# Kernel optimization log

Hardware: AMD Instinct MI355X
Metric: run time of the kernel (lower is better)

## Reference

```python
import jax, jax.numpy as jnp
import numpy as np

B, C, H, W, K = 8, 768, 64, 64, 256
EPS = 1e-12  # torch F.normalize eps


def setup_inputs() -> dict:
    key = jax.random.key(0)
    k1, k2 = jax.random.split(key)
    return {
        "x": jax.random.normal(k1, (B, C, H, W), dtype=jnp.float32),
        "centroids": jax.random.normal(k2, (B, C, K), dtype=jnp.float32),
        "sim_alpha": jnp.ones((1,), dtype=jnp.float32),
        "sim_beta": jnp.zeros((1,), dtype=jnp.float32),
    }


def reference(x, centroids, sim_alpha, sim_beta):
    b, c, h, w = x.shape
    n = h * w
    x_r = x.reshape(b, c, n)               # (B,C,N)
    xt = jnp.swapaxes(x_r, 1, 2)           # (B,N,C) tokens
    ct = jnp.swapaxes(centroids, 1, 2)     # (B,K,C) centroids
    # cosine similarity (F.normalize uses max(norm, eps))
    xn = xt / jnp.maximum(jnp.linalg.norm(xt, axis=-1, keepdims=True), EPS)
    cn = ct / jnp.maximum(jnp.linalg.norm(ct, axis=-1, keepdims=True), EPS)
    cos = jnp.einsum('bkc,bnc->bkn', cn, xn)                  # (B,K,N)
    sim = jax.nn.sigmoid(sim_beta + sim_alpha * cos)          # (B,K,N)
    # hard assignment mask: each token kept only for its argmax centroid
    max_idx = jnp.argmax(sim, axis=1)                         # (B,N)
    mask = jnp.swapaxes(jax.nn.one_hot(max_idx, sim.shape[1], dtype=sim.dtype), 1, 2)  # (B,K,N)
    sim_masked = sim * mask                                   # (B,K,N)
    # aggregation: sum over tokens weighted by masked similarity
    agg = jnp.einsum('bkn,bnc->bkc', sim_masked, xt)          # (B,K,C)
    counts = jnp.sum(mask, axis=-1, keepdims=True)            # (B,K,1)
    hyperedges = (agg + ct) / (counts + 1.0)                  # (B,K,C)
    return hyperedges, sim_masked
```

## Files before the change

kernel.cpp:

```cpp
#include <hip/hip_runtime.h>
#include <cmath>

#define Bdim 8
#define Cdim 768
#define Kdim 256
#define Ndim 4096
#define NT 64
#define KC2 32
#define NCH (Cdim / KC2)

typedef __bf16 bf16x8 __attribute__((ext_vector_type(8)));
typedef short  s16x8  __attribute__((ext_vector_type(8)));
typedef float  f32x4  __attribute__((ext_vector_type(4)));
union U8 { s16x8 s; bf16x8 b; };

typedef __attribute__((address_space(1))) const unsigned int g_u32;
typedef __attribute__((address_space(3))) unsigned int l_u32;
__device__ __forceinline__ void gload16(const void* g, void* l) {
    __builtin_amdgcn_global_load_lds((g_u32*)g, (l_u32*)l, 16, 0, 0);
}

__device__ __forceinline__ unsigned short bf16_rne(float f) {
    unsigned u = __float_as_uint(f);
    unsigned r = u + 0x7FFFu + ((u >> 16) & 1u);
    return (unsigned short)(r >> 16);
}
__device__ __forceinline__ float bf2f(unsigned short h) {
    return __uint_as_float((unsigned)h << 16);
}

__device__ __forceinline__ void split3(float v, short& h, short& m, short& l) {
    unsigned u = __float_as_uint(v);
    unsigned th = u + 0x7FFFu + ((u >> 16) & 1u);
    h = (short)(th >> 16);
    float r1 = v - __uint_as_float(th & 0xFFFF0000u);
    unsigned u1 = __float_as_uint(r1);
    unsigned tm = u1 + 0x7FFFu + ((u1 >> 16) & 1u);
    m = (short)(tm >> 16);
    float r2 = r1 - __uint_as_float(tm & 0xFFFF0000u);
    unsigned u2 = __float_as_uint(r2);
    unsigned tl = u2 + 0x7FFFu + ((u2 >> 16) & 1u);
    l = (short)(tl >> 16);
}

__global__ __launch_bounds__(256) void prep_kernel(
    const float* __restrict__ cents, float* __restrict__ invc, int* __restrict__ cnt)
{
    __shared__ float red[4][Kdim];
    const int tid = threadIdx.x;
    const int b = blockIdx.x;
    const float* cb = cents + (size_t)b * Cdim * Kdim;
    const int q = tid & 63, g = tid >> 6;
    float4 ss = make_float4(0.f, 0.f, 0.f, 0.f);
    for (int r = g; r < Cdim; r += 4) {
        float4 v = *(const float4*)(cb + (size_t)r * Kdim + q * 4);
        ss.x = fmaf(v.x, v.x, ss.x); ss.y = fmaf(v.y, v.y, ss.y);
        ss.z = fmaf(v.z, v.z, ss.z); ss.w = fmaf(v.w, v.w, ss.w);
    }
    *(float4*)&red[g][q * 4] = ss;
    __syncthreads();
    float s = red[0][tid] + red[1][tid] + red[2][tid] + red[3][tid];
    invc[b * Kdim + tid] = 1.f / fmaxf(sqrtf(s), 1e-12f);
    cnt[b * Kdim + tid] = 0;
}

__global__ __launch_bounds__(256) void cvt_kernel(
    const float* __restrict__ cents, short* __restrict__ centH,
    short* __restrict__ centM, short* __restrict__ centL)
{
    const int k = threadIdx.x;
    const int bc = blockIdx.x;
    const float* src = cents + ((size_t)(bc / 96) * Cdim + (size_t)(bc % 96) * 8) * Kdim + k;
    s16x8 H, M, L;
    #pragma unroll
    for (int e = 0; e < 8; ++e) {
        short h, m, l;
        split3(src[(size_t)e * Kdim], h, m, l);
        H[e] = h; M[e] = m; L[e] = l;
    }
    ((s16x8*)centH)[(size_t)bc * 256 + k] = H;
    ((s16x8*)centM)[(size_t)bc * 256 + k] = M;
    ((s16x8*)centL)[(size_t)bc * 256 + k] = L;
}

__global__ __launch_bounds__(256) void cvt2_kernel(
    const float* __restrict__ cents, short* __restrict__ centH,
    short* __restrict__ centM, short* __restrict__ centL,
    float* __restrict__ csq)
{
    const int k = threadIdx.x;
    const int bc = blockIdx.x;
    const float* src = cents + ((size_t)(bc / 96) * Cdim + (size_t)(bc % 96) * 8) * Kdim + k;
    s16x8 H, M, L;
    float sq = 0.f;
    #pragma unroll
    for (int e = 0; e < 8; ++e) {
        float v = src[(size_t)e * Kdim];
        sq = fmaf(v, v, sq);
        short h, m, l;
        split3(v, h, m, l);
        H[e] = h; M[e] = m; L[e] = l;
    }
    ((s16x8*)centH)[(size_t)bc * 256 + k] = H;
    ((s16x8*)centM)[(size_t)bc * 256 + k] = M;
    ((s16x8*)centL)[(size_t)bc * 256 + k] = L;
    csq[(size_t)bc * 256 + k] = sq;
}

__global__ __launch_bounds__(256) void nrm_reduce_kernel(
    const float* __restrict__ csq, float* __restrict__ invc, int* __restrict__ cnt)
{
    const int k = threadIdx.x;
    const int b = blockIdx.x;
    const float* p = csq + (size_t)b * 96 * 256 + k;
    float s0 = 0.f, s1 = 0.f, s2 = 0.f, s3 = 0.f;
    #pragma unroll
    for (int j = 0; j < 96; j += 4) {
        s0 += p[(j + 0) * 256];
        s1 += p[(j + 1) * 256];
        s2 += p[(j + 2) * 256];
        s3 += p[(j + 3) * 256];
    }
    float s = ((s0 + s1) + (s2 + s3));
    invc[b * Kdim + k] = 1.f / fmaxf(sqrtf(s), 1e-12f);
    cnt[b * Kdim + k] = 0;
}

__global__ __launch_bounds__(256) void xpose3_kernel(
    const float* __restrict__ x,
    unsigned short* __restrict__ xH, unsigned short* __restrict__ xM,
    unsigned short* __restrict__ xL, float* __restrict__ xn2p)
{
    __shared__ float tile[64][68];
    __shared__ float psum[4][64];
    const int tid = threadIdx.x;
    const int bid = blockIdx.x;
    const int b  = bid / (12 * 64);
    const int r  = bid % (12 * 64);
    const int ct = r / 64, nt = r % 64;
    const float* src = x + ((size_t)b * Cdim + ct * 64) * Ndim + nt * 64;
    #pragma unroll
    for (int it = 0; it < 4; ++it) {
        int idx = tid + it * 256;
        int c = idx >> 4, n4 = idx & 15;
        *(float4*)&tile[c][n4 * 4] = *(const float4*)&src[(size_t)c * Ndim + n4 * 4];
    }
    __syncthreads();

    {
        const int grp = tid >> 6, tn = tid & 63;
        float s = 0.f;
        #pragma unroll
        for (int cc = 0; cc < 16; ++cc) {
            float v = tile[grp * 16 + cc][tn];
            s = fmaf(v, v, s);
        }
        psum[grp][tn] = s;
    }
    __syncthreads();
    if (tid < 64)
        xn2p[((size_t)(b * 12 + ct)) * Ndim + nt * 64 + tid] =
            psum[0][tid] + psum[1][tid] + psum[2][tid] + psum[3][tid];

    #pragma unroll
    for (int it = 0; it < 8; ++it) {
        int idx = tid + it * 256;
        int n = idx >> 5, cp = idx & 31;
        short h0, m0, l0, h1, m1, l1;
        split3(tile[cp * 2][n],     h0, m0, l0);
        split3(tile[cp * 2 + 1][n], h1, m1, l1);
        size_t o = ((size_t)(b * Ndim + nt * 64 + n)) * Cdim + ct * 64 + cp * 2;
        *(unsigned*)&xH[o] = (unsigned)(unsigned short)h0 | ((unsigned)(unsigned short)h1 << 16);
        *(unsigned*)&xM[o] = (unsigned)(unsigned short)m0 | ((unsigned)(unsigned short)m1 << 16);
        *(unsigned*)&xL[o] = (unsigned)(unsigned short)l0 | ((unsigned)(unsigned short)l1 << 16);
    }
}

__global__ __launch_bounds__(256) void xpose_kernel(
    const float* __restrict__ x, unsigned short* __restrict__ xTh)
{
    __shared__ float tile[64][68];
    const int tid = threadIdx.x;
    const int bid = blockIdx.x;
    const int b  = bid / (12 * 64);
    const int r  = bid % (12 * 64);
    const int ct = r / 64, nt = r % 64;
    const float* src = x + ((size_t)b * Cdim + ct * 64) * Ndim + nt * 64;
    #pragma unroll
    for (int it = 0; it < 4; ++it) {
        int idx = tid + it * 256;
        int c = idx >> 4, n4 = idx & 15;
        *(float4*)&tile[c][n4 * 4] = *(const float4*)&src[(size_t)c * Ndim + n4 * 4];
    }
    __syncthreads();
    #pragma unroll
    for (int it = 0; it < 8; ++it) {
        int idx = tid + it * 256;
        int n = idx >> 5, cp = idx & 31;
        unsigned pk = (unsigned)bf16_rne(tile[cp * 2][n])
                    | ((unsigned)bf16_rne(tile[cp * 2 + 1][n]) << 16);
        *(unsigned*)&xTh[((size_t)(b * Ndim + nt * 64 + n)) * Cdim + ct * 64 + cp * 2] = pk;
    }
}

__global__ __launch_bounds__(256) void scan_kernel(
    const int* __restrict__ cnt, const int* __restrict__ kArr,
    int* __restrict__ bucketOff, int* __restrict__ toks)
{
    __shared__ int cS[256];
    __shared__ int offS[256];
    __shared__ int cur[256];
    const int tid = threadIdx.x;
    const int b = blockIdx.x;
    cS[tid] = cnt[b * 256 + tid];
    __syncthreads();
    if (tid == 0) {
        int a = 0;
        for (int k = 0; k < 256; ++k) { offS[k] = a; a += cS[k]; }
    }
    __syncthreads();
    bucketOff[b * 256 + tid] = offS[tid];
    cur[tid] = offS[tid];
    __syncthreads();
    for (int i = tid; i < Ndim; i += 256) {
        int k = kArr[b * Ndim + i];
        int pos = atomicAdd(&cur[k], 1);
        toks[b * Ndim + pos] = i;
    }
}

__global__ __launch_bounds__(192) void aggB_kernel(
    const unsigned short* __restrict__ xTh,
    const float* __restrict__ cents,
    const float* __restrict__ wArr,
    const int* __restrict__ toks,
    const int* __restrict__ bucketOff,
    const int* __restrict__ cnt,
    float* __restrict__ hyp)
{
    const int tid = threadIdx.x;
    const int b  = blockIdx.x >> 7;
    const int kg = blockIdx.x & 127;
    const int t4 = tid * 4;
    #pragma unroll
    for (int j = 0; j < 2; ++j) {
        const int k = kg * 2 + j;
        const int off = bucketOff[b * 256 + k];
        const int num = cnt[b * 256 + k];
        const int base = b * Ndim + off;
        float a0 = 0.f, a1 = 0.f, a2 = 0.f, a3 = 0.f;
        int i = 0;
        for (; i + 4 <= num; i += 4) {
            int na = toks[base + i],     nb = toks[base + i + 1];
            int nc = toks[base + i + 2], nd = toks[base + i + 3];
            float wa = wArr[b * Ndim + na], wb = wArr[b * Ndim + nb];
            float wc = wArr[b * Ndim + nc], wd = wArr[b * Ndim + nd];
            ushort4 ha = *(const ushort4*)&xTh[((size_t)(b * Ndim + na)) * Cdim + t4];
            ushort4 hb = *(const ushort4*)&xTh[((size_t)(b * Ndim + nb)) * Cdim + t4];
            ushort4 hc = *(const ushort4*)&xTh[((size_t)(b * Ndim + nc)) * Cdim + t4];
            ushort4 hd = *(const ushort4*)&xTh[((size_t)(b * Ndim + nd)) * Cdim + t4];
            a0 += wa * bf2f(ha.x) + wb * bf2f(hb.x) + wc * bf2f(hc.x) + wd * bf2f(hd.x);
            a1 += wa * bf2f(ha.y) + wb * bf2f(hb.y) + wc * bf2f(hc.y) + wd * bf2f(hd.y);
            a2 += wa * bf2f(ha.z) + wb * bf2f(hb.z) + wc * bf2f(hc.z) + wd * bf2f(hd.z);
            a3 += wa * bf2f(ha.w) + wb * bf2f(hb.w) + wc * bf2f(hc.w) + wd * bf2f(hd.w);
        }
        for (; i < num; ++i) {
            int n = toks[base + i];
            float w = wArr[b * Ndim + n];
            ushort4 h = *(const ushort4*)&xTh[((size_t)(b * Ndim + n)) * Cdim + t4];
            a0 += w * bf2f(h.x); a1 += w * bf2f(h.y);
            a2 += w * bf2f(h.z); a3 += w * bf2f(h.w);
        }
        float d = (float)(num + 1);
        float4 o;
        o.x = (a0 + cents[((size_t)b * Cdim + t4 + 0) * Kdim + k]) / d;
        o.y = (a1 + cents[((size_t)b * Cdim + t4 + 1) * Kdim + k]) / d;
        o.z = (a2 + cents[((size_t)b * Cdim + t4 + 2) * Kdim + k]) / d;
        o.w = (a3 + cents[((size_t)b * Cdim + t4 + 3) * Kdim + k]) / d;
        *(float4*)&hyp[((size_t)(b * Kdim + k)) * Cdim + t4] = o;
    }
}

#define PASS(Afr, Bfr)                                                        \
    _Pragma("unroll")                                                         \
    for (int kf = 0; kf < 4; ++kf)                                            \
        _Pragma("unroll")                                                     \
        for (int nf = 0; nf < 4; ++nf)                                        \
            acc[kf][nf] = __builtin_amdgcn_mfma_f32_16x16x32_bf16(            \
                Afr[kf].b, Bfr[nf].b, acc[kf][nf], 0, 0, 0);

__global__ __launch_bounds__(256, 2) void sim_stage_kernel(
    const short* __restrict__ xH, const short* __restrict__ xM,
    const short* __restrict__ xL,
    const short* __restrict__ centH, const short* __restrict__ centM,
    const short* __restrict__ centL,
    const float* __restrict__ alpha_p, const float* __restrict__ beta_p,
    const float* __restrict__ invc, const float* __restrict__ xn2p,
    float* __restrict__ simOut, float* __restrict__ wArr,
    int* __restrict__ kArr, int* __restrict__ cnt)
{
    __shared__ __align__(16) s16x8 sB[3][3][256];
    __shared__ float bwv[4][NT];
    __shared__ int   bwk[4][NT];

    const int tid  = threadIdx.x;
    const int lane = tid & 63;
    const int w    = tid >> 6;
    const int q    = lane >> 4;
    const int c15  = lane & 15;
    const int b    = blockIdx.x >> 6;
    const int n0   = (blockIdx.x & 63) * NT;

    const int nloc = w * 16 + (lane >> 2);
    const int rsw  = (lane & 3) ^ ((nloc >> 1) & 3);
    const size_t gsrc = ((size_t)b * Ndim + n0 + nloc) * 96 + rsw;
    const s16x8* xHp = (const s16x8*)xH;
    const s16x8* xMp = (const s16x8*)xM;
    const s16x8* xLp = (const s16x8*)xL;

    #define STAGE(t_) do { const int bf_ = (t_) % 3;                          \
        gload16(xHp + gsrc + (size_t)(t_) * 4, &sB[bf_][0][w * 64]);          \
        gload16(xMp + gsrc + (size_t)(t_) * 4, &sB[bf_][1][w * 64]);          \
        gload16(xLp + gsrc + (size_t)(t_) * 4, &sB[bf_][2][w * 64]);          \
    } while (0)

    const s16x8* cHb = (const s16x8*)centH + (size_t)b * 96 * 256;
    const s16x8* cMb = (const s16x8*)centM + (size_t)b * 96 * 256;
    const s16x8* cLb = (const s16x8*)centL + (size_t)b * 96 * 256;
    const int rowA0 = w * 64 + c15;

    f32x4 acc[4][4];
    #pragma unroll
    for (int i = 0; i < 4; ++i)
        #pragma unroll
        for (int j = 0; j < 4; ++j) acc[i][j] = (f32x4){0.f, 0.f, 0.f, 0.f};

    STAGE(0);
    STAGE(1);

    const int swz = (c15 >> 1) & 3;

    for (int t = 0; t < NCH; ++t) {
        asm volatile("s_waitcnt vmcnt(3)" ::: "memory");
        __builtin_amdgcn_s_barrier();
        __builtin_amdgcn_sched_barrier(0);

        const int cur = t % 3;

        U8 aH[4], aM[4], aL[4];
        {
            const int ra = (t * 4 + q) * 256 + rowA0;
            #pragma unroll
            for (int kf = 0; kf < 4; ++kf) {
                aH[kf].s = cHb[ra + kf * 16];
                aM[kf].s = cMb[ra + kf * 16];
                aL[kf].s = cLb[ra + kf * 16];
            }
        }
        if (t + 2 < NCH) STAGE(t + 2);

        U8 bH[4], bM[4], bL[4];
        #pragma unroll
        for (int nf = 0; nf < 4; ++nf) {
            const int ri = (nf * 16 + c15) * 4 + (q ^ swz);
            bH[nf].s = sB[cur][0][ri];
            bM[nf].s = sB[cur][1][ri];
            bL[nf].s = sB[cur][2][ri];
        }

        PASS(aH, bH) PASS(aM, bH) PASS(aL, bH)
        PASS(aH, bM) PASS(aM, bM) PASS(aH, bL)
    }
    #undef STAGE

    const float alpha = alpha_p[0];
    const float beta  = beta_p[0];

    #pragma unroll
    for (int nf = 0; nf < 4; ++nf) {
        const int n = n0 + nf * 16 + c15;
        float xs = 0.f;
        #pragma unroll
        for (int j = 0; j < 12; ++j) xs += xn2p[(size_t)(b * 12 + j) * Ndim + n];
        const float ivx = 1.f / fmaxf(sqrtf(xs), 1e-12f);
        float best = -1.f; int bk = 0;
        #pragma unroll
        for (int kf = 0; kf < 4; ++kf) {
            float4 ic = *(const float4*)&invc[b * Kdim + w * 64 + kf * 16 + q * 4];
            #pragma unroll
            for (int r = 0; r < 4; ++r) {
                float cosv = acc[kf][nf][r] * ((const float*)&ic)[r] * ivx;
                float s = 1.f / (1.f + expf(-(beta + alpha * cosv)));
                int k = w * 64 + kf * 16 + q * 4 + r;
                if (s > best) { best = s; bk = k; }
            }
        }
        #pragma unroll
        for (int off = 16; off < 64; off <<= 1) {
            float ov = __shfl_xor(best, off);
            int   ok = __shfl_xor(bk, off);
            if (ov > best || (ov == best && ok < bk)) { best = ov; bk = ok; }
        }
        if (q == 0) { bwv[w][nf * 16 + c15] = best; bwk[w][nf * 16 + c15] = bk; }
    }
    __syncthreads();
    if (tid < NT) {
        float best = -1.f; int bk = 0;
        #pragma unroll
        for (int g = 0; g < 4; ++g) {
            float v = bwv[g][tid];
            if (v > best) { best = v; bk = bwk[g][tid]; }
        }
        int gn = b * Ndim + n0 + tid;
        wArr[gn] = best;
        kArr[gn] = bk;
        simOut[((size_t)(b * Kdim + bk)) * Ndim + n0 + tid] = best;
        atomicAdd(&cnt[b * Kdim + bk], 1);
    }
}

__global__ __launch_bounds__(256, 2) void sim_mfma_kernel(
    const float* __restrict__ x,
    const short* __restrict__ centH,
    const short* __restrict__ centM,
    const short* __restrict__ centL,
    const float* __restrict__ alpha_p,
    const float* __restrict__ beta_p,
    const float* __restrict__ invc,
    float* __restrict__ simOut,
    float* __restrict__ wArr,
    int*   __restrict__ kArr,
    int*   __restrict__ cnt)
{
    __shared__ __align__(16) float sxf[3][KC2][NT];
    __shared__ float invcS[Kdim];
    __shared__ float px[4][NT];
    __shared__ float invxS[NT];
    __shared__ float bwv[4][NT];
    __shared__ int   bwk[4][NT];

    const int tid  = threadIdx.x;
    const int lane = tid & 63;
    const int w    = tid >> 6;
    const int q    = lane >> 4;
    const int c15  = lane & 15;
    const int b    = blockIdx.x >> 6;
    const int n0   = (blockIdx.x & 63) * NT;
    const float* xb = x + (size_t)b * Cdim * Ndim;

    invcS[tid] = invc[b * Kdim + tid];
    const float alpha = alpha_p[0];
    const float beta  = beta_p[0];

    f32x4 acc[4][4];
    #pragma unroll
    for (int i = 0; i < 4; ++i)
        #pragma unroll
        for (int j = 0; j < 4; ++j) acc[i][j] = (f32x4){0.f, 0.f, 0.f, 0.f};

    float xn2p_ = 0.f;

    #define STAGE(t_) do {                                                    \
        const int bf_ = (t_) % 3; const int c0_ = (t_) * KC2;                 \
        _Pragma("unroll")                                                     \
        for (int i_ = 0; i_ < 2; ++i_)                                        \
            gload16(xb + (size_t)(c0_ + w * 8 + i_ * 4 + q) * Ndim            \
                       + n0 + c15 * 4,                                        \
                    &sxf[bf_][w * 8 + i_ * 4][0]);                            \
    } while (0)

    STAGE(0);
    STAGE(1);

    const s16x8* cHb = (const s16x8*)centH + ((size_t)b * 96) * 256;
    const s16x8* cMb = (const s16x8*)centM + ((size_t)b * 96) * 256;
    const s16x8* cLb = (const s16x8*)centL + ((size_t)b * 96) * 256;

    for (int t = 0; t < NCH; ++t) {
        asm volatile("s_waitcnt vmcnt(2)" ::: "memory");
        __builtin_amdgcn_s_barrier();
        __builtin_amdgcn_sched_barrier(0);

        const int cur = t % 3;

        U8 aH[4], aM[4], aL[4];
        {
            const size_t rowb = ((size_t)(t * 4 + q)) * 256 + w * 64 + c15;
            #pragma unroll
            for (int kf = 0; kf < 4; ++kf) {
                aH[kf].s = cHb[rowb + kf * 16];
                aM[kf].s = cMb[rowb + kf * 16];
                aL[kf].s = cLb[rowb + kf * 16];
            }
        }
        if (t + 2 < NCH) STAGE(t + 2);

        #pragma unroll
        for (int r = 0; r < 8; ++r) {
            float v = sxf[cur][w * 8 + r][lane];
            xn2p_ = fmaf(v, v, xn2p_);
        }

        U8 bH[4], bM[4], bL[4];
        #pragma unroll
        for (int nf = 0; nf < 4; ++nf) {
            #pragma unroll
            for (int e = 0; e < 8; ++e) {
                short h, m, l;
                split3(sxf[cur][q * 8 + e][nf * 16 + c15], h, m, l);
                bH[nf].s[e] = h; bM[nf].s[e] = m; bL[nf].s[e] = l;
            }
        }

        PASS(aH, bH) PASS(aH, bM) PASS(aM, bH)
        PASS(aH, bL) PASS(aL, bH) PASS(aM, bM)
    }
    #undef STAGE

    __syncthreads();
    px[w][lane] = xn2p_;
    __syncthreads();
    if (tid < NT) {
        float s = px[0][tid] + px[1][tid] + px[2][tid] + px[3][tid];
        invxS[tid] = 1.f / fmaxf(sqrtf(s), 1e-12f);
    }
    __syncthreads();

    #pragma unroll
    for (int nf = 0; nf < 4; ++nf) {
        const float ivx = invxS[nf * 16 + c15];
        float best = -1.f; int bk = 0;
        #pragma unroll
        for (int kf = 0; kf < 4; ++kf) {
            float4 ic = *(const float4*)&invcS[w * 64 + kf * 16 + q * 4];
            #pragma unroll
            for (int r = 0; r < 4; ++r) {
                float cosv = acc[kf][nf][r] * ((const float*)&ic)[r] * ivx;
                float s = 1.f / (1.f + expf(-(beta + alpha * cosv)));
                int k = w * 64 + kf * 16 + q * 4 + r;
                if (s > best) { best = s; bk = k; }
            }
        }
        #pragma unroll
        for (int off = 16; off < 64; off <<= 1) {
            float ov = __shfl_xor(best, off);
            int   ok = __shfl_xor(bk, off);
            if (ov > best || (ov == best && ok < bk)) { best = ov; bk = ok; }
        }
        if (q == 0) { bwv[w][nf * 16 + c15] = best; bwk[w][nf * 16 + c15] = bk; }
    }
    __syncthreads();
    if (tid < NT) {
        float best = -1.f; int bk = 0;
        #pragma unroll
        for (int g = 0; g < 4; ++g) {
            float v = bwv[g][tid];
            if (v > best) { best = v; bk = bwk[g][tid]; }
        }
        int gn = b * Ndim + n0 + tid;
        wArr[gn] = best;
        kArr[gn] = bk;
        simOut[((size_t)(b * Kdim + bk)) * Ndim + n0 + tid] = best;
        atomicAdd(&cnt[b * Kdim + bk], 1);
    }
}

extern "C" void kernel_launch(void* const* d_in, const int* in_sizes, int n_in,
                              void* d_out, int out_size, void* d_ws, size_t ws_size,
                              hipStream_t stream)
{
    const float* x     = (const float*)d_in[0];
    const float* cents = (const float*)d_in[1];
    const float* alpha = (const float*)d_in[2];
    const float* beta  = (const float*)d_in[3];

    float* hyp    = (float*)d_out;
    float* simOut = (float*)d_out + (size_t)Bdim * Kdim * Cdim;

    char* ws = (char*)d_ws;
    hipMemsetAsync(simOut, 0, (size_t)Bdim * Kdim * Ndim * sizeof(float), stream);

    const size_t WS_FULL = 163209216ull;
    const size_t WS_R13  = 60186624ull;

    if (ws_size >= WS_FULL) {
        float* wArr  = (float*)(ws);
        int*   kArr  = (int*)  (ws + 131072);
        int*   cnt   = (int*)  (ws + 262144);
        float* invc  = (float*)(ws + 270336);
        float* xn2p  = (float*)(ws + 278528);
        short* centH = (short*)(ws + 1851392);
        short* centM = (short*)(ws + 4997120);
        short* centL = (short*)(ws + 8142848);
        int*   toks  = (int*)  (ws + 11288576);
        int*   boff  = (int*)  (ws + 11419648);
        unsigned short* xH = (unsigned short*)(ws + 11427840);
        unsigned short* xM = (unsigned short*)(ws + 61759488);
        unsigned short* xL = (unsigned short*)(ws + 112091136);
        float* csq   = (float*)(ws + 162422784);

        cvt2_kernel<<<dim3(Bdim * 96), dim3(256), 0, stream>>>(
            cents, centH, centM, centL, csq);
        nrm_reduce_kernel<<<dim3(Bdim), dim3(256), 0, stream>>>(csq, invc, cnt);
        xpose3_kernel<<<dim3(Bdim * 12 * 64), dim3(256), 0, stream>>>(x, xH, xM, xL, xn2p);
        sim_stage_kernel<<<dim3(Bdim * (Ndim / NT)), dim3(256), 0, stream>>>(
            (const short*)xH, (const short*)xM, (const short*)xL,
            centH, centM, centL, alpha, beta, invc, xn2p,
            simOut, wArr, kArr, cnt);
        scan_kernel<<<dim3(Bdim), dim3(256), 0, stream>>>(cnt, kArr, boff, toks);
        aggB_kernel<<<dim3(Bdim * 128), dim3(192), 0, stream>>>(
            xH, cents, wArr, toks, boff, cnt, hyp);
    } else if (ws_size >= WS_R13) {
        float* wArr  = (float*)(ws);
        int*   kArr  = (int*)  (ws + 131072);
        int*   cnt   = (int*)  (ws + 262144);
        float* invc  = (float*)(ws + 270336);
        short* centH = (short*)(ws + 278528);
        short* centM = (short*)(ws + 3424256);
        short* centL = (short*)(ws + 6569984);
        int*   toks  = (int*)  (ws + 9715712);
        int*   boff  = (int*)  (ws + 9846784);
        unsigned short* xTh = (unsigned short*)(ws + 9854976);

        prep_kernel<<<dim3(Bdim), dim3(256), 0, stream>>>(cents, invc, cnt);
        cvt_kernel<<<dim3(Bdim * 96), dim3(256), 0, stream>>>(cents, centH, centM, centL);
        xpose_kernel<<<dim3(Bdim * 12 * 64), dim3(256), 0, stream>>>(x, xTh);
        sim_mfma_kernel<<<dim3(Bdim * (Ndim / NT)), dim3(256), 0, stream>>>(
            x, centH, centM, centL, alpha, beta, invc, simOut, wArr, kArr, cnt);
        scan_kernel<<<dim3(Bdim), dim3(256), 0, stream>>>(cnt, kArr, boff, toks);
        aggB_kernel<<<dim3(Bdim * 128), dim3(192), 0, stream>>>(
            xTh, cents, wArr, toks, boff, cnt, hyp);
    }
}
```

Measured before the change: 171.2 us.

## Halve sim-stage token tile to 32 and raise occupancy with reorganized staging

```diff
diff --git a/kernel.cpp b/kernel.cpp
--- a/kernel.cpp
+++ b/kernel.cpp
@@ -6,6 +6,7 @@
 #define Kdim 256
 #define Ndim 4096
 #define NT 64
+#define NT2 32
 #define KC2 32
 #define NCH (Cdim / KC2)
 
@@ -281,6 +282,14 @@
     }
 }
 
+#define PASS2(Afr, Bfr)                                                       \
+    _Pragma("unroll")                                                         \
+    for (int kf = 0; kf < 4; ++kf)                                            \
+        _Pragma("unroll")                                                     \
+        for (int nf = 0; nf < 2; ++nf)                                        \
+            acc[kf][nf] = __builtin_amdgcn_mfma_f32_16x16x32_bf16(            \
+                Afr[kf].b, Bfr[nf].b, acc[kf][nf], 0, 0, 0);
+
 #define PASS(Afr, Bfr)                                                        \
     _Pragma("unroll")                                                         \
     for (int kf = 0; kf < 4; ++kf)                                            \
@@ -289,7 +298,7 @@
             acc[kf][nf] = __builtin_amdgcn_mfma_f32_16x16x32_bf16(            \
                 Afr[kf].b, Bfr[nf].b, acc[kf][nf], 0, 0, 0);
 
-__global__ __launch_bounds__(256, 2) void sim_stage_kernel(
+__global__ __launch_bounds__(256, 4) void sim_stage32_kernel(
     const short* __restrict__ xH, const short* __restrict__ xM,
     const short* __restrict__ xL,
     const short* __restrict__ centH, const short* __restrict__ centM,
@@ -299,29 +308,29 @@
     float* __restrict__ simOut, float* __restrict__ wArr,
     int* __restrict__ kArr, int* __restrict__ cnt)
 {
-    __shared__ __align__(16) s16x8 sB[3][3][256];
-    __shared__ float bwv[4][NT];
-    __shared__ int   bwk[4][NT];
+    __shared__ __align__(16) s16x8 sB[3][3][128];
+    __shared__ float bwv[4][NT2];
+    __shared__ int   bwk[4][NT2];
 
     const int tid  = threadIdx.x;
     const int lane = tid & 63;
     const int w    = tid >> 6;
     const int q    = lane >> 4;
     const int c15  = lane & 15;
-    const int b    = blockIdx.x >> 6;
-    const int n0   = (blockIdx.x & 63) * NT;
-
-    const int nloc = w * 16 + (lane >> 2);
-    const int rsw  = (lane & 3) ^ ((nloc >> 1) & 3);
-    const size_t gsrc = ((size_t)b * Ndim + n0 + nloc) * 96 + rsw;
-    const s16x8* xHp = (const s16x8*)xH;
-    const s16x8* xMp = (const s16x8*)xM;
-    const s16x8* xLp = (const s16x8*)xL;
+    const int b    = blockIdx.x & 7;
+    const int n0   = (blockIdx.x >> 3) * NT2;
+
+    const int we = (w == 3) ? 0 : w;
+    const s16x8* myplane = (we == 0) ? (const s16x8*)xH
+                         : (we == 1) ? (const s16x8*)xM : (const s16x8*)xL;
+    const int nl0 = (lane >> 2);
+    const int nl1 = 16 + (lane >> 2);
+    const size_t gs0 = ((size_t)b * Ndim + n0 + nl0) * 96 + ((lane & 3) ^ ((nl0 >> 1) & 3));
+    const size_t gs1 = ((size_t)b * Ndim + n0 + nl1) * 96 + ((lane & 3) ^ ((nl1 >> 1) & 3));
 
     #define STAGE(t_) do { const int bf_ = (t_) % 3;                          \
-        gload16(xHp + gsrc + (size_t)(t_) * 4, &sB[bf_][0][w * 64]);          \
-        gload16(xMp + gsrc + (size_t)(t_) * 4, &sB[bf_][1][w * 64]);          \
-        gload16(xLp + gsrc + (size_t)(t_) * 4, &sB[bf_][2][w * 64]);          \
+        gload16(myplane + gs0 + (size_t)(t_) * 4, &sB[bf_][we][0]);           \
+        gload16(myplane + gs1 + (size_t)(t_) * 4, &sB[bf_][we][64]);          \
     } while (0)
 
     const s16x8* cHb = (const s16x8*)centH + (size_t)b * 96 * 256;
@@ -329,11 +338,11 @@
     const s16x8* cLb = (const s16x8*)centL + (size_t)b * 96 * 256;
     const int rowA0 = w * 64 + c15;
 
-    f32x4 acc[4][4];
+    f32x4 acc[4][2];
     #pragma unroll
     for (int i = 0; i < 4; ++i)
         #pragma unroll
-        for (int j = 0; j < 4; ++j) acc[i][j] = (f32x4){0.f, 0.f, 0.f, 0.f};
+        for (int j = 0; j < 2; ++j) acc[i][j] = (f32x4){0.f, 0.f, 0.f, 0.f};
 
     STAGE(0);
     STAGE(1);
@@ -341,7 +350,7 @@
     const int swz = (c15 >> 1) & 3;
 
     for (int t = 0; t < NCH; ++t) {
-        asm volatile("s_waitcnt vmcnt(3)" ::: "memory");
+        asm volatile("s_waitcnt vmcnt(2)" ::: "memory");
         __builtin_amdgcn_s_barrier();
         __builtin_amdgcn_sched_barrier(0);
 
@@ -359,17 +368,17 @@
         }
         if (t + 2 < NCH) STAGE(t + 2);
 
-        U8 bH[4], bM[4], bL[4];
-        #pragma unroll
-        for (int nf = 0; nf < 4; ++nf) {
+        U8 bH[2], bM[2], bL[2];
+        #pragma unroll
+        for (int nf = 0; nf < 2; ++nf) {
             const int ri = (nf * 16 + c15) * 4 + (q ^ swz);
             bH[nf].s = sB[cur][0][ri];
             bM[nf].s = sB[cur][1][ri];
             bL[nf].s = sB[cur][2][ri];
         }
 
-        PASS(aH, bH) PASS(aM, bH) PASS(aL, bH)
-        PASS(aH, bM) PASS(aM, bM) PASS(aH, bL)
+        PASS2(aH, bH) PASS2(aM, bH) PASS2(aL, bH)
+        PASS2(aH, bM) PASS2(aM, bM) PASS2(aH, bL)
     }
     #undef STAGE
 
@@ -377,7 +386,7 @@
     const float beta  = beta_p[0];
 
     #pragma unroll
-    for (int nf = 0; nf < 4; ++nf) {
+    for (int nf = 0; nf < 2; ++nf) {
         const int n = n0 + nf * 16 + c15;
         float xs = 0.f;
         #pragma unroll
@@ -404,7 +413,7 @@
         if (q == 0) { bwv[w][nf * 16 + c15] = best; bwk[w][nf * 16 + c15] = bk; }
     }
     __syncthreads();
-    if (tid < NT) {
+    if (tid < NT2) {
         float best = -1.f; int bk = 0;
         #pragma unroll
         for (int g = 0; g < 4; ++g) {
@@ -603,7 +612,7 @@
             cents, centH, centM, centL, csq);
         nrm_reduce_kernel<<<dim3(Bdim), dim3(256), 0, stream>>>(csq, invc, cnt);
         xpose3_kernel<<<dim3(Bdim * 12 * 64), dim3(256), 0, stream>>>(x, xH, xM, xL, xn2p);
-        sim_stage_kernel<<<dim3(Bdim * (Ndim / NT)), dim3(256), 0, stream>>>(
+        sim_stage32_kernel<<<dim3(Bdim * (Ndim / NT2)), dim3(256), 0, stream>>>(
             (const short*)xH, (const short*)xM, (const short*)xL,
             centH, centM, centL, alpha, beta, invc, xn2p,
             simOut, wArr, kArr, cnt);
```

After: 174.8 us. +2.1%, slower.

## Prefetch centroid fragments one chunk ahead and remap blocks batch-interleaved

Applied to the files above, without the earlier changes.

```diff
diff --git a/kernel.cpp b/kernel.cpp
--- a/kernel.cpp
+++ b/kernel.cpp
@@ -308,8 +308,8 @@
     const int w    = tid >> 6;
     const int q    = lane >> 4;
     const int c15  = lane & 15;
-    const int b    = blockIdx.x >> 6;
-    const int n0   = (blockIdx.x & 63) * NT;
+    const int b    = blockIdx.x & 7;
+    const int n0   = (blockIdx.x >> 3) * NT;
 
     const int nloc = w * 16 + (lane >> 2);
     const int rsw  = (lane & 3) ^ ((nloc >> 1) & 3);
@@ -329,48 +329,59 @@
     const s16x8* cLb = (const s16x8*)centL + (size_t)b * 96 * 256;
     const int rowA0 = w * 64 + c15;
 
+    #define LOADA(dstH, dstM, dstL, t_) do {                                  \
+        const int ra_ = ((t_) * 4 + q) * 256 + rowA0;                         \
+        _Pragma("unroll")                                                     \
+        for (int kf = 0; kf < 4; ++kf) {                                      \
+            dstH[kf].s = cHb[ra_ + kf * 16];                                  \
+            dstM[kf].s = cMb[ra_ + kf * 16];                                  \
+            dstL[kf].s = cLb[ra_ + kf * 16];                                  \
+        }                                                                     \
+    } while (0)
+
     f32x4 acc[4][4];
     #pragma unroll
     for (int i = 0; i < 4; ++i)
         #pragma unroll
         for (int j = 0; j < 4; ++j) acc[i][j] = (f32x4){0.f, 0.f, 0.f, 0.f};
 
+    U8 aH0[4], aM0[4], aL0[4];
+    U8 aH1[4], aM1[4], aL1[4];
+
+    LOADA(aH0, aM0, aL0, 0);
     STAGE(0);
     STAGE(1);
 
     const int swz = (c15 >> 1) & 3;
 
-    for (int t = 0; t < NCH; ++t) {
-        asm volatile("s_waitcnt vmcnt(3)" ::: "memory");
-        __builtin_amdgcn_s_barrier();
-        __builtin_amdgcn_sched_barrier(0);
-
-        const int cur = t % 3;
-
-        U8 aH[4], aM[4], aL[4];
-        {
-            const int ra = (t * 4 + q) * 256 + rowA0;
-            #pragma unroll
-            for (int kf = 0; kf < 4; ++kf) {
-                aH[kf].s = cHb[ra + kf * 16];
-                aM[kf].s = cMb[ra + kf * 16];
-                aL[kf].s = cLb[ra + kf * 16];
-            }
-        }
-        if (t + 2 < NCH) STAGE(t + 2);
-
-        U8 bH[4], bM[4], bL[4];
-        #pragma unroll
-        for (int nf = 0; nf < 4; ++nf) {
-            const int ri = (nf * 16 + c15) * 4 + (q ^ swz);
-            bH[nf].s = sB[cur][0][ri];
-            bM[nf].s = sB[cur][1][ri];
-            bL[nf].s = sB[cur][2][ri];
-        }
-
-        PASS(aH, bH) PASS(aM, bH) PASS(aL, bH)
-        PASS(aH, bM) PASS(aM, bM) PASS(aH, bL)
-    }
+    #define CHUNK(t_, aHc, aMc, aLc, aHn, aMn, aLn)                           \
+    {                                                                         \
+        asm volatile("s_waitcnt vmcnt(3)" ::: "memory");                      \
+        __builtin_amdgcn_s_barrier();                                         \
+        __builtin_amdgcn_sched_barrier(0);                                    \
+        { const int tn_ = ((t_) + 1 < NCH) ? (t_) + 1 : NCH - 1;              \
+          LOADA(aHn, aMn, aLn, tn_); }                                        \
+        __builtin_amdgcn_sched_barrier(0);                                    \
+        if ((t_) + 2 < NCH) STAGE((t_) + 2);                                  \
+        const int cur_ = (t_) % 3;                                            \
+        U8 bH[4], bM[4], bL[4];                                               \
+        _Pragma("unroll")                                                     \
+        for (int nf = 0; nf < 4; ++nf) {                                      \
+            const int ri = (nf * 16 + c15) * 4 + (q ^ swz);                   \
+            bH[nf].s = sB[cur_][0][ri];                                       \
+            bM[nf].s = sB[cur_][1][ri];                                       \
+            bL[nf].s = sB[cur_][2][ri];                                       \
+        }                                                                     \
+        PASS(aHc, bH) PASS(aMc, bH) PASS(aLc, bH)                             \
+        PASS(aHc, bM) PASS(aMc, bM) PASS(aHc, bL)                             \
+    }
+
+    for (int t = 0; t < NCH; t += 2) {
+        CHUNK(t,     aH0, aM0, aL0, aH1, aM1, aL1);
+        CHUNK(t + 1, aH1, aM1, aL1, aH0, aM0, aL0);
+    }
+    #undef CHUNK
+    #undef LOADA
     #undef STAGE
 
     const float alpha = alpha_p[0];
```

Result: no change. 170.4 us (median of 2 runs) (-0.5%).
